# Optimization experiments

Hardware: AMD Instinct MI355X
Metric: run time of the kernel (lower is better)

Reference implementation:

```python
import jax, jax.numpy as jnp
import numpy as np

NUM_HEAD = 4
HIDDEN = 128
NEG = 9e15


def _mha(x, maskf, wq, bq, wk, bk, wv, bv, wo, bo):
    # DGN-style multi-head attention: relu on q/k/v projections, mask-multiplied
    # scores with -9e15 fill on masked entries, relu on output projection.
    bs, n, _ = x.shape
    dh = HIDDEN // NUM_HEAD
    def proj(w, b):
        return jax.nn.relu(x @ w.T + b).reshape(bs, n, NUM_HEAD, dh).transpose(0, 2, 1, 3)
    q, k, v = proj(wq, bq), proj(wk, bk), proj(wv, bv)  # [bs,H,n,dh]
    scores = jnp.einsum('bhnd,bhmd->bhnm', q, k) / jnp.sqrt(jnp.asarray(dh, x.dtype))
    m = maskf[:, None]  # [bs,1,n,n]
    scores = scores * m - NEG * (1.0 - m)
    att = jax.nn.softmax(scores, axis=-1)
    out = jnp.einsum('bhnm,bhmd->bhnd', att, v).transpose(0, 2, 1, 3).reshape(bs, n, HIDDEN)
    return jax.nn.relu(out @ wo.T + bo), att


def _gru_cell(xin, h, w_ih, w_hh, b_ih, b_hh):
    gi = xin @ w_ih.T + b_ih  # [N, 3*hidden]
    gh = h @ w_hh.T + b_hh
    i_r, i_z, i_n = jnp.split(gi, 3, axis=-1)
    h_r, h_z, h_n = jnp.split(gh, 3, axis=-1)
    r = jax.nn.sigmoid(i_r + h_r)
    z = jax.nn.sigmoid(i_z + h_z)
    n = jnp.tanh(i_n + r * h_n)
    return (1.0 - z) * n + z * h


def setup_inputs() -> dict:
    key = jax.random.key(0)
    ks = jax.random.split(key, 20)
    bs, n_ant, in_dim, hd, act = 4096, 64, 64, 128, 20
    s = 0.05
    x = jax.random.normal(ks[0], (bs, n_ant, in_dim), jnp.float32)
    mask = jax.random.randint(ks[1], (bs, n_ant, n_ant), 0, 2, jnp.int32)
    eye = jnp.eye(n_ant, dtype=jnp.int32)[None]
    mask = jnp.maximum(mask, eye)  # ensure self-edges so no softmax row is fully masked
    hidden_state = jax.random.normal(ks[2], (bs, n_ant, hd), jnp.float32)
    def w(k, shape):
        return jax.random.normal(k, shape, jnp.float32) * s
    return dict(
        x=x, mask=mask, hidden_state=hidden_state,
        enc_w=w(ks[3], (hd, in_dim)), enc_b=jnp.zeros((hd,), jnp.float32),
        q1_w=w(ks[4], (hd, hd)), q1_b=jnp.zeros((hd,), jnp.float32),
        k1_w=w(ks[5], (hd, hd)), k1_b=jnp.zeros((hd,), jnp.float32),
        v1_w=w(ks[6], (hd, hd)), v1_b=jnp.zeros((hd,), jnp.float32),
        o1_w=w(ks[7], (hd, hd)), o1_b=jnp.zeros((hd,), jnp.float32),
        q2_w=w(ks[8], (hd, hd)), q2_b=jnp.zeros((hd,), jnp.float32),
        k2_w=w(ks[9], (hd, hd)), k2_b=jnp.zeros((hd,), jnp.float32),
        v2_w=w(ks[10], (hd, hd)), v2_b=jnp.zeros((hd,), jnp.float32),
        o2_w=w(ks[11], (hd, hd)), o2_b=jnp.zeros((hd,), jnp.float32),
        gru_w_ih=w(ks[12], (3 * hd, hd)), gru_w_hh=w(ks[13], (3 * hd, hd)),
        gru_b_ih=jnp.zeros((3 * hd,), jnp.float32), gru_b_hh=jnp.zeros((3 * hd,), jnp.float32),
        lin_w=w(ks[14], (act, hd)), lin_b=jnp.zeros((act,), jnp.float32),
    )


def reference(x, mask, hidden_state,
              enc_w, enc_b,
              q1_w, q1_b, k1_w, k1_b, v1_w, v1_b, o1_w, o1_b,
              q2_w, q2_b, k2_w, k2_b, v2_w, v2_b, o2_w, o2_b,
              gru_w_ih, gru_w_hh, gru_b_ih, gru_b_hh,
              lin_w, lin_b):
    bs, n_ant, _ = x.shape
    maskf = mask.astype(x.dtype)
    xe = jax.nn.relu(x @ enc_w.T + enc_b)                     # [bs,n,hidden]
    h1, _ = _mha(xe, maskf, q1_w, q1_b, k1_w, k1_b, v1_w, v1_b, o1_w, o1_b)
    h2, _ = _mha(h1, maskf, q2_w, q2_b, k2_w, k2_b, v2_w, v2_b, o2_w, o2_b)
    h2f = h2.reshape(bs * n_ant, HIDDEN)
    hf = hidden_state.reshape(bs * n_ant, HIDDEN)
    h3 = _gru_cell(h2f, hf, gru_w_ih, gru_w_hh, gru_b_ih, gru_b_hh).reshape(bs, n_ant, HIDDEN)
    qs = h3 @ lin_w.T + lin_b                                 # with_non_linearity=False
    return qs, h3
```

## Files before the change

kernel.cpp:

```cpp
#include <hip/hip_runtime.h>
#include <hip/hip_bf16.h>

typedef unsigned int u32;
typedef unsigned short u16;
typedef unsigned long long u64;

using bf16x8 = __attribute__((ext_vector_type(8))) short;
using f32x4  = __attribute__((ext_vector_type(4))) float;
typedef float f4v __attribute__((ext_vector_type(4)));

#define NUNITS 31
#define WS_BIAS_OFF (NUNITS*8192)
#define NBIAS 1952

__device__ __forceinline__ u32 pk2(float a, float b){
    __hip_bfloat162 h = __float22bfloat162_rn(make_float2(a, b));
    union { __hip_bfloat162 h2; u32 u; } cv; cv.h2 = h; return cv.u;
}
__device__ __forceinline__ float b2f(u16 v){ return __uint_as_float(((u32)v) << 16); }
__device__ __forceinline__ int swch(int chunk, int key){ return (chunk & ~7) | ((chunk ^ key) & 7); }

__global__ __launch_bounds__(256) void convert_weights(
    const float* __restrict__ enc_w,
    const float* __restrict__ q1, const float* __restrict__ k1,
    const float* __restrict__ v1, const float* __restrict__ o1,
    const float* __restrict__ q2, const float* __restrict__ k2,
    const float* __restrict__ v2, const float* __restrict__ o2,
    const float* __restrict__ gih, const float* __restrict__ ghh,
    const float* __restrict__ lin,
    const float* __restrict__ enc_b,
    const float* __restrict__ q1b, const float* __restrict__ k1b,
    const float* __restrict__ v1b, const float* __restrict__ o1b,
    const float* __restrict__ q2b, const float* __restrict__ k2b,
    const float* __restrict__ v2b, const float* __restrict__ o2b,
    const float* __restrict__ gbih, const float* __restrict__ gbhh,
    const float* __restrict__ linb,
    u16* __restrict__ dst)
{
    int idx = blockIdx.x*256 + threadIdx.x;
    if (idx < NUNITS*8192){
        int u = idx >> 13, rem = idx & 8191;
        int w = rem >> 11;
        int t = (rem >> 9) & 3;
        int l = (rem >> 3) & 63;
        int e = idx & 7;
        int i = t >> 1, kk = t & 1;
        int oc = (w*2 + i)*16 + (l & 15);
        int kl = kk*32 + (l >> 4)*8 + e;
        float val;
        if (u == 0){
            val = enc_w[oc*64 + kl];
        } else if (u <= 16){
            int v = u - 1; int L = v >> 3; int r8 = v & 7;
            int mat, kh;
            if (r8 < 6){ mat = r8 % 3; kh = r8 / 3; } else { mat = 3; kh = r8 - 6; }
            const float* s;
            if (L == 0){ s = (mat==0)?q1:(mat==1)?k1:(mat==2)?v1:o1; }
            else       { s = (mat==0)?q2:(mat==1)?k2:(mat==2)?v2:o2; }
            val = s[oc*128 + kh*64 + kl];
        } else if (u <= 28){
            int v = u - 17;
            int gate, kh; const float* s;
            if (v < 8){ gate = v & 1; kh = (v >> 1) & 1; s = (v >= 4) ? ghh : gih; }
            else      { int w8 = v - 8; gate = 2; kh = w8 & 1; s = (w8 >= 2) ? ghh : gih; }
            val = s[(gate*128 + oc)*128 + kh*64 + kl];
        } else {
            int kh = u - 29;
            val = (oc < 20) ? lin[oc*128 + kh*64 + kl] : 0.f;
        }
        __hip_bfloat16 hv = __float2bfloat16(val);
        union { __hip_bfloat16 h; u16 us; } cv; cv.h = hv;
        dst[idx] = cv.us;
    } else if (idx < NUNITS*8192 + NBIAS){
        int i = idx - NUNITS*8192;
        float val;
        if      (i < 128)  val = enc_b[i];
        else if (i < 256)  val = q1b[i-128];
        else if (i < 384)  val = k1b[i-256];
        else if (i < 512)  val = v1b[i-384];
        else if (i < 640)  val = o1b[i-512];
        else if (i < 768)  val = q2b[i-640];
        else if (i < 896)  val = k2b[i-768];
        else if (i < 1024) val = v2b[i-896];
        else if (i < 1152) val = o2b[i-1024];
        else if (i < 1536) val = gbih[i-1152];
        else if (i < 1920) val = gbhh[i-1536];
        else if (i < 1940) val = linb[i-1920];
        else               val = 0.f;
        ((float*)(dst + NUNITS*8192))[i] = val;
    }
}

#define BARX() do{ asm volatile("s_waitcnt lgkmcnt(0)" ::: "memory"); \
                   __builtin_amdgcn_s_barrier(); \
                   asm volatile("" ::: "memory"); }while(0)

struct WB { bf16x8 a[4]; };

template<int U>
__device__ __forceinline__ WB load_unit(const u16* Wu, int w, int lane){
    const u16* p = Wu + U*8192 + w*2048 + lane*8;
    WB b;
    b.a[0] = *(const bf16x8*)(p);
    b.a[1] = *(const bf16x8*)(p + 512);
    b.a[2] = *(const bf16x8*)(p + 1024);
    b.a[3] = *(const bf16x8*)(p + 1536);
    return b;
}

template<int M,int N>
__device__ __forceinline__ void zacc(f32x4 (&a)[M][N]){
    #pragma unroll
    for (int i=0;i<M;i++)
        #pragma unroll
        for (int j=0;j<N;j++) a[i][j] = (f32x4){0.f,0.f,0.f,0.f};
}

struct XF { bf16x8 f[4][2]; };

__device__ __forceinline__ void loadX(XF& xf, const u16* X, int kh, int c, int g){
    const int key = c & 7;
    #pragma unroll
    for (int kk = 0; kk < 2; kk++){
        const int pw = (kk*4 + g) ^ key;
        #pragma unroll
        for (int j = 0; j < 4; j++)
            xf.f[j][kk] = *(const bf16x8*)(X + (j*16 + c)*128 + (kh*8 + pw)*8);
    }
}

__device__ __forceinline__ void wgemmW(const WB& wb, const XF& xf, f32x4 (&acc)[2][4]){
    __builtin_amdgcn_s_setprio(1);
    #pragma unroll
    for (int kk = 0; kk < 2; kk++){
        #pragma unroll
        for (int j = 0; j < 4; j++){
            acc[0][j] = __builtin_amdgcn_mfma_f32_16x16x32_bf16(wb.a[kk],   xf.f[j][kk], acc[0][j], 0,0,0);
            acc[1][j] = __builtin_amdgcn_mfma_f32_16x16x32_bf16(wb.a[2+kk], xf.f[j][kk], acc[1][j], 0,0,0);
        }
    }
    __builtin_amdgcn_s_setprio(0);
}

__device__ __forceinline__ void vgemmW(const WB& wb, const XF& xf, f32x4 (&acc)[4][2]){
    __builtin_amdgcn_s_setprio(1);
    #pragma unroll
    for (int kk = 0; kk < 2; kk++){
        #pragma unroll
        for (int i = 0; i < 4; i++){
            acc[i][0] = __builtin_amdgcn_mfma_f32_16x16x32_bf16(xf.f[i][kk], wb.a[kk],   acc[i][0], 0,0,0);
            acc[i][1] = __builtin_amdgcn_mfma_f32_16x16x32_bf16(xf.f[i][kk], wb.a[2+kk], acc[i][1], 0,0,0);
        }
    }
    __builtin_amdgcn_s_setprio(0);
}

__device__ __forceinline__ void epiW(f32x4 (&acc)[2][4], float4 bv0, float4 bv1,
                                     u16* dst, int w, int c, int g){
    const int key = c & 7;
    #pragma unroll
    for (int i = 0; i < 2; i++){
        float4 bv = i ? bv1 : bv0;
        const int col0 = (w*2+i)*16 + g*4;
        const int coff = swch(col0>>3, key)*8 + (col0&7);
        #pragma unroll
        for (int j = 0; j < 4; j++){
            int row = j*16 + c;
            float v0 = fmaxf(acc[i][j][0]+bv.x, 0.f);
            float v1 = fmaxf(acc[i][j][1]+bv.y, 0.f);
            float v2 = fmaxf(acc[i][j][2]+bv.z, 0.f);
            float v3 = fmaxf(acc[i][j][3]+bv.w, 0.f);
            uint2 o; o.x = pk2(v0,v1); o.y = pk2(v2,v3);
            *(uint2*)(dst + row*128 + coff) = o;
        }
    }
}

template<int LAYER>
__device__ __forceinline__ void mha_layer(const u16* Wu,
                                          u16* ACT, u16* QXp, u16* KPp,
                                          const float* wsb, const float* h0, size_t rowbase,
                                          int tid, int w, int lane, int c, int g, const u64* mbits)
{
    constexpr int UB = 1 + LAYER*8;
    constexpr int BB = 128 + LAYER*512;
    const int key = c & 7;
    const int col00 = w*32 + g*4;
    const int col01 = col00 + 16;

    XF xf;
    f32x4 accQ[2][4], accK[2][4];
    f32x4 vacc[4][2];

    WB b_q0 = load_unit<UB+0>(Wu, w, lane);
    WB b_k0 = load_unit<UB+1>(Wu, w, lane);
    WB b_v0 = load_unit<UB+2>(Wu, w, lane);

    zacc(accQ); zacc(accK); zacc(vacc);
    loadX(xf, ACT, 0, c, g);
    wgemmW(b_q0, xf, accQ);
    WB b_q1 = load_unit<UB+3>(Wu, w, lane);
    wgemmW(b_k0, xf, accK);
    WB b_k1 = load_unit<UB+4>(Wu, w, lane);
    vgemmW(b_v0, xf, vacc);
    WB b_v1 = load_unit<UB+5>(Wu, w, lane);

    loadX(xf, ACT, 1, c, g);
    float4 bq0 = *(const float4*)(wsb + BB + col00);
    float4 bq1 = *(const float4*)(wsb + BB + col01);
    wgemmW(b_q1, xf, accQ);
    WB b_o0 = load_unit<UB+6>(Wu, w, lane);
    epiW(accQ, bq0, bq1, QXp, w, c, g);

    float4 bk0 = *(const float4*)(wsb + BB + 128 + col00);
    float4 bk1 = *(const float4*)(wsb + BB + 128 + col01);
    wgemmW(b_k1, xf, accK);
    WB b_o1 = load_unit<UB+7>(Wu, w, lane);
    epiW(accK, bk0, bk1, KPp, w, c, g);

    float bv0 = wsb[BB + 256 + w*32 + c];
    float bv1 = wsb[BB + 256 + w*32 + 16 + c];
    vgemmW(b_v1, xf, vacc);

    BARX();

    #pragma unroll
    for (int j = 0; j < 2; j++){
        int vrow = w*32 + j*16 + c;
        float bv = j ? bv1 : bv0;
        #pragma unroll
        for (int i = 0; i < 4; i++){
            int kk = i >> 1, p = i & 1;
            float v0 = fmaxf(vacc[i][j][0]+bv, 0.f);
            float v1 = fmaxf(vacc[i][j][1]+bv, 0.f);
            float v2 = fmaxf(vacc[i][j][2]+bv, 0.f);
            float v3 = fmaxf(vacc[i][j][3]+bv, 0.f);
            uint2 o; o.x = pk2(v0,v1); o.y = pk2(v2,v3);
            *(uint2*)(ACT + vrow*64 + swch(kk*4+g, key)*8 + p*4) = o;
        }
    }

    const int h = w;
    f32x4 sc[4][4];
    {
        bf16x8 kf[4];
        #pragma unroll
        for (int kt = 0; kt < 4; kt++)
            kf[kt] = *(const bf16x8*)(KPp + (kt*16 + c)*128 + swch(h*4+g, key)*8);
        __builtin_amdgcn_s_setprio(1);
        #pragma unroll
        for (int qt = 0; qt < 4; qt++){
            bf16x8 qf = *(const bf16x8*)(QXp + (qt*16 + c)*128 + swch(h*4+g, key)*8);
            #pragma unroll
            for (int kt = 0; kt < 4; kt++){
                f32x4 z4 = (f32x4){0.f,0.f,0.f,0.f};
                sc[qt][kt] = __builtin_amdgcn_mfma_f32_16x16x32_bf16(kf[kt], qf, z4, 0,0,0);
            }
        }
        __builtin_amdgcn_s_setprio(0);
    }

    f4v hr[8];
    if (LAYER == 1){
        const float* hp = h0 + (rowbase + (tid>>2))*128 + (tid&3)*32;
        #pragma unroll
        for (int t = 0; t < 8; t++)
            hr[t] = __builtin_nontemporal_load((const f4v*)(hp + t*4));
    }

    {
        u32 pp[4][4][2];
        #pragma unroll
        for (int qt = 0; qt < 4; qt++){
            u64 mb = mbits[qt];
            float mx = -1e30f;
            #pragma unroll
            for (int kt = 0; kt < 4; kt++)
                #pragma unroll
                for (int r = 0; r < 4; r++){
                    float s = sc[qt][kt][r] * 0.17677669529663687f;
                    s = ((mb >> (kt*16 + g*4 + r)) & 1ull) ? s : -1e30f;
                    sc[qt][kt][r] = s;
                    mx = fmaxf(mx, s);
                }
            mx = fmaxf(mx, __shfl_xor(mx, 16));
            mx = fmaxf(mx, __shfl_xor(mx, 32));
            float sum = 0.f;
            #pragma unroll
            for (int kt = 0; kt < 4; kt++)
                #pragma unroll
                for (int r = 0; r < 4; r++){
                    float e = __expf(sc[qt][kt][r] - mx);
                    sc[qt][kt][r] = e; sum += e;
                }
            sum += __shfl_xor(sum, 16);
            sum += __shfl_xor(sum, 32);
            float inv = 1.f / sum;
            #pragma unroll
            for (int kt = 0; kt < 4; kt++){
                pp[qt][kt][0] = pk2(sc[qt][kt][0]*inv, sc[qt][kt][1]*inv);
                pp[qt][kt][1] = pk2(sc[qt][kt][2]*inv, sc[qt][kt][3]*inv);
            }
        }
        #pragma unroll
        for (int dt = 0; dt < 2; dt++){
            f32x4 pa[4];
            #pragma unroll
            for (int qt = 0; qt < 4; qt++) pa[qt] = (f32x4){0.f,0.f,0.f,0.f};
            #pragma unroll
            for (int kk = 0; kk < 2; kk++){
                bf16x8 vt = *(const bf16x8*)(ACT + (h*32 + dt*16 + c)*64 + ((kk*4+g)^key)*8);
                __builtin_amdgcn_s_setprio(1);
                #pragma unroll
                for (int qt = 0; qt < 4; qt++){
                    union { u32 u4[4]; bf16x8 v8; } bbv;
                    bbv.u4[0]=pp[qt][kk*2][0];   bbv.u4[1]=pp[qt][kk*2][1];
                    bbv.u4[2]=pp[qt][kk*2+1][0]; bbv.u4[3]=pp[qt][kk*2+1][1];
                    pa[qt] = __builtin_amdgcn_mfma_f32_16x16x32_bf16(vt, bbv.v8, pa[qt], 0,0,0);
                }
                __builtin_amdgcn_s_setprio(0);
            }
            #pragma unroll
            for (int qt = 0; qt < 4; qt++){
                int col = h*32 + dt*16 + g*4;
                uint2 o; o.x = pk2(pa[qt][0], pa[qt][1]); o.y = pk2(pa[qt][2], pa[qt][3]);
                *(uint2*)(QXp + (qt*16 + c)*128 + swch(col>>3, key)*8 + (col&7)) = o;
            }
        }
    }

    BARX();

    if (LAYER == 1){
        int hrow = tid >> 2, seg = tid & 3;
        #pragma unroll
        for (int cc = 0; cc < 4; cc++){
            int p = seg*4 + cc;
            int ps = (p & 8) | ((p ^ (hrow & 7)) & 7);
            f4v fa = hr[cc*2], fb = hr[cc*2+1];
            uint4 o; o.x = pk2(fa.x,fa.y); o.y = pk2(fa.z,fa.w);
            o.z = pk2(fb.x,fb.y); o.w = pk2(fb.z,fb.w);
            *(uint4*)(KPp + hrow*128 + ps*8) = o;
        }
    }

    f32x4 acc[2][4];
    zacc(acc);
    loadX(xf, QXp, 0, c, g);
    wgemmW(b_o0, xf, acc);
    WB b_n0 = load_unit<UB+8>(Wu, w, lane);
    loadX(xf, QXp, 1, c, g);
    float4 bo0 = *(const float4*)(wsb + BB + 384 + col00);
    float4 bo1 = *(const float4*)(wsb + BB + 384 + col01);
    wgemmW(b_o1, xf, acc);
    WB b_n1 = load_unit<UB+9>(Wu, w, lane);
    epiW(acc, bo0, bo1, ACT, w, c, g);
    asm volatile("" :: "v"(b_n0.a[0]), "v"(b_n1.a[0]));

    BARX();
}

__global__ __launch_bounds__(256, 2) void drgn_pipe(
    const float* __restrict__ x, const int* __restrict__ maskg,
    const float* __restrict__ h0, const u16* __restrict__ W16,
    float* __restrict__ out_qs, float* __restrict__ out_h3)
{
    __shared__ __align__(16) u16 SMEM[24576];
    u16* ACT = SMEM;
    u16* QXp = SMEM + 8192;
    u16* KPp = SMEM + 16384;

    const int tid = threadIdx.x;
    const int w = tid >> 6, lane = tid & 63;
    const int c = lane & 15, g = lane >> 4;
    const int key = c & 7;
    const size_t rowbase = (size_t)blockIdx.x * 64;
    const u16* Wu = W16;
    const float* wsb = (const float*)(W16 + WS_BIAS_OFF);
    const int col00 = w*32 + g*4;
    const int col01 = col00 + 16;

    u64* MrowT = (u64*)KPp;
    #pragma unroll 4
    for (int rr = 0; rr < 16; rr++){
        int row = w*16 + rr;
        int mv = __builtin_nontemporal_load(maskg + (rowbase + row)*64 + lane);
        u64 bits = __ballot(mv != 0);
        if (lane == 0) MrowT[row] = bits;
    }
    for (int i = tid; i < 512; i += 256){
        int row = i >> 3, p = i & 7;
        int lc = (p ^ (row & 7)) & 7;
        const float* sp = x + (rowbase + row)*64 + lc*8;
        f4v f0 = __builtin_nontemporal_load((const f4v*)sp);
        f4v f1 = __builtin_nontemporal_load((const f4v*)(sp + 4));
        uint4 o; o.x = pk2(f0.x,f0.y); o.y = pk2(f0.z,f0.w);
        o.z = pk2(f1.x,f1.y); o.w = pk2(f1.z,f1.w);
        *(uint4*)(QXp + row*128 + p*8) = o;
    }
    WB b_enc = load_unit<0>(Wu, w, lane);
    __syncthreads();
    u64 mbits[4];
    #pragma unroll
    for (int qt = 0; qt < 4; qt++) mbits[qt] = MrowT[qt*16 + c];

    {
        XF xf;
        f32x4 acc[2][4];
        float4 b0 = *(const float4*)(wsb + col00);
        float4 b1 = *(const float4*)(wsb + col01);
        zacc(acc);
        loadX(xf, QXp, 0, c, g);
        wgemmW(b_enc, xf, acc);
        epiW(acc, b0, b1, ACT, w, c, g);
    }
    BARX();

    mha_layer<0>(Wu, ACT, QXp, KPp, wsb, h0, rowbase, tid, w, lane, c, g, mbits);
    mha_layer<1>(Wu, ACT, QXp, KPp, wsb, h0, rowbase, tid, w, lane, c, g, mbits);

    XF xf;
    float rrA[2][4][4], zzA[2][4][4];
    {
        f32x4 aIr[2][4], aIz[2][4], aHr[2][4], aHz[2][4];
        WB g17 = load_unit<17>(Wu, w, lane);
        WB g18 = load_unit<18>(Wu, w, lane);
        zacc(aIr); zacc(aIz);
        loadX(xf, ACT, 0, c, g);
        wgemmW(g17, xf, aIr);
        WB g19 = load_unit<19>(Wu, w, lane);
        wgemmW(g18, xf, aIz);
        WB g20 = load_unit<20>(Wu, w, lane);
        loadX(xf, ACT, 1, c, g);
        wgemmW(g19, xf, aIr);
        WB g21 = load_unit<21>(Wu, w, lane);
        wgemmW(g20, xf, aIz);
        WB g22 = load_unit<22>(Wu, w, lane);
        zacc(aHr); zacc(aHz);
        loadX(xf, KPp, 0, c, g);
        wgemmW(g21, xf, aHr);
        WB g23 = load_unit<23>(Wu, w, lane);
        wgemmW(g22, xf, aHz);
        WB g24 = load_unit<24>(Wu, w, lane);
        loadX(xf, KPp, 1, c, g);
        wgemmW(g23, xf, aHr);
        wgemmW(g24, xf, aHz);

        float4 bir0 = *(const float4*)(wsb + 1152 + col00);
        float4 bir1 = *(const float4*)(wsb + 1152 + col01);
        float4 bhr0 = *(const float4*)(wsb + 1536 + col00);
        float4 bhr1 = *(const float4*)(wsb + 1536 + col01);
        float4 biz0 = *(const float4*)(wsb + 1152 + 128 + col00);
        float4 biz1 = *(const float4*)(wsb + 1152 + 128 + col01);
        float4 bhz0 = *(const float4*)(wsb + 1536 + 128 + col00);
        float4 bhz1 = *(const float4*)(wsb + 1536 + 128 + col01);
        #pragma unroll
        for (int i = 0; i < 2; i++){
            float4 bir = i ? bir1 : bir0; float4 bhr = i ? bhr1 : bhr0;
            float4 biz = i ? biz1 : biz0; float4 bhz = i ? bhz1 : bhz0;
            #pragma unroll
            for (int j = 0; j < 4; j++)
                #pragma unroll
                for (int r = 0; r < 4; r++){
                    rrA[i][j][r] = 1.f/(1.f + __expf(-(aIr[i][j][r] + (&bir.x)[r] + aHr[i][j][r] + (&bhr.x)[r])));
                    zzA[i][j][r] = 1.f/(1.f + __expf(-(aIz[i][j][r] + (&biz.x)[r] + aHz[i][j][r] + (&bhz.x)[r])));
                }
        }
    }
    WB g29, g30;
    {
        f32x4 aIn[2][4], aHn[2][4];
        WB g25 = load_unit<25>(Wu, w, lane);
        WB g26 = load_unit<26>(Wu, w, lane);
        zacc(aIn);
        loadX(xf, ACT, 0, c, g);
        wgemmW(g25, xf, aIn);
        WB g27 = load_unit<27>(Wu, w, lane);
        loadX(xf, ACT, 1, c, g);
        wgemmW(g26, xf, aIn);
        WB g28 = load_unit<28>(Wu, w, lane);
        zacc(aHn);
        loadX(xf, KPp, 0, c, g);
        wgemmW(g27, xf, aHn);
        g29 = load_unit<29>(Wu, w, lane);
        loadX(xf, KPp, 1, c, g);
        wgemmW(g28, xf, aHn);
        g30 = load_unit<30>(Wu, w, lane);

        float4 bin0 = *(const float4*)(wsb + 1152 + 256 + col00);
        float4 bin1 = *(const float4*)(wsb + 1152 + 256 + col01);
        float4 bhn0 = *(const float4*)(wsb + 1536 + 256 + col00);
        float4 bhn1 = *(const float4*)(wsb + 1536 + 256 + col01);

        BARX();

        #pragma unroll
        for (int i = 0; i < 2; i++){
            float4 bi = i ? bin1 : bin0; float4 bh = i ? bhn1 : bhn0;
            int col0 = w*32 + i*16 + g*4;
            int coff = swch(col0>>3, key)*8 + (col0&7);
            #pragma unroll
            for (int j = 0; j < 4; j++){
                int row = j*16 + c;
                uint2 hv = *(const uint2*)(KPp + row*128 + coff);
                float h0v[4] = { b2f((u16)(hv.x & 0xffffu)), b2f((u16)(hv.x >> 16)),
                                 b2f((u16)(hv.y & 0xffffu)), b2f((u16)(hv.y >> 16)) };
                f4v h3o;
                #pragma unroll
                for (int r = 0; r < 4; r++){
                    float xn = aIn[i][j][r] + (&bi.x)[r] + rrA[i][j][r]*(aHn[i][j][r] + (&bh.x)[r]);
                    float e2 = __expf(-2.f*fabsf(xn));
                    float th = (1.f - e2)/(1.f + e2);
                    th = (xn >= 0.f) ? th : -th;
                    float zv = zzA[i][j][r];
                    h3o[r] = (1.f - zv)*th + zv*h0v[r];
                }
                uint2 o; o.x = pk2(h3o[0],h3o[1]); o.y = pk2(h3o[2],h3o[3]);
                *(uint2*)(ACT + row*128 + coff) = o;
                __builtin_nontemporal_store(h3o, (f4v*)(out_h3 + (rowbase + row)*128 + col0));
            }
        }
    }
    BARX();

    {
        f32x4 qa[2][4];
        float4 lb0 = (col00 < 20) ? *(const float4*)(wsb + 1920 + col00) : (float4){0.f,0.f,0.f,0.f};
        float4 lb1 = (col01 < 20) ? *(const float4*)(wsb + 1920 + col01) : (float4){0.f,0.f,0.f,0.f};
        zacc(qa);
        loadX(xf, ACT, 0, c, g);
        wgemmW(g29, xf, qa);
        loadX(xf, ACT, 1, c, g);
        wgemmW(g30, xf, qa);

        #pragma unroll
        for (int i = 0; i < 2; i++){
            int col0 = w*32 + i*16 + g*4;
            if (col0 < 20){
                float4 lb = i ? lb1 : lb0;
                #pragma unroll
                for (int j = 0; j < 4; j++){
                    int row = j*16 + c;
                    f4v o;
                    o.x = qa[i][j][0]+lb.x; o.y = qa[i][j][1]+lb.y;
                    o.z = qa[i][j][2]+lb.z; o.w = qa[i][j][3]+lb.w;
                    __builtin_nontemporal_store(o, (f4v*)(out_qs + (rowbase + row)*20 + col0));
                }
            }
        }
    }
}

extern "C" void kernel_launch(void* const* d_in, const int* in_sizes, int n_in,
                              void* d_out, int out_size, void* d_ws, size_t ws_size,
                              hipStream_t stream) {
    const float* x     = (const float*)d_in[0];
    const int*   mask  = (const int*)  d_in[1];
    const float* h0    = (const float*)d_in[2];
    const float* enc_w = (const float*)d_in[3];
    const float* enc_b = (const float*)d_in[4];
    const float* q1_w  = (const float*)d_in[5];  const float* q1_b = (const float*)d_in[6];
    const float* k1_w  = (const float*)d_in[7];  const float* k1_b = (const float*)d_in[8];
    const float* v1_w  = (const float*)d_in[9];  const float* v1_b = (const float*)d_in[10];
    const float* o1_w  = (const float*)d_in[11]; const float* o1_b = (const float*)d_in[12];
    const float* q2_w  = (const float*)d_in[13]; const float* q2_b = (const float*)d_in[14];
    const float* k2_w  = (const float*)d_in[15]; const float* k2_b = (const float*)d_in[16];
    const float* v2_w  = (const float*)d_in[17]; const float* v2_b = (const float*)d_in[18];
    const float* o2_w  = (const float*)d_in[19]; const float* o2_b = (const float*)d_in[20];
    const float* gwih  = (const float*)d_in[21]; const float* gwhh = (const float*)d_in[22];
    const float* gbih  = (const float*)d_in[23]; const float* gbhh = (const float*)d_in[24];
    const float* lin_w = (const float*)d_in[25]; const float* lin_b = (const float*)d_in[26];

    const int bs = in_sizes[0] / (64 * 64);
    float* out_qs = (float*)d_out;
    float* out_h3 = out_qs + (size_t)bs * 64 * 20;
    u16* W16 = (u16*)d_ws;

    const int total = NUNITS*8192 + NBIAS;
    hipLaunchKernelGGL(convert_weights, dim3((total + 255) / 256), dim3(256), 0, stream,
                       enc_w, q1_w, k1_w, v1_w, o1_w, q2_w, k2_w, v2_w, o2_w,
                       gwih, gwhh, lin_w,
                       enc_b, q1_b, k1_b, v1_b, o1_b, q2_b, k2_b, v2_b, o2_b,
                       gbih, gbhh, lin_b, W16);
    hipLaunchKernelGGL(drgn_pipe, dim3(bs), dim3(256), 0, stream,
                       x, mask, h0, W16, out_qs, out_h3);
}
```

Baseline: 328.8 us.

## Prefetch next-layer weights across stages, fold softmax scale, use fast exp2/rcp

Weight units for the next stage (layer 1 QKV, GRU first units) are now loaded at the end of the previous stage and passed through, so global weight latency overlaps the preceding GEMMs. The softmax drops the max-subtraction pass by pre-scaling Q with scale*log2e and using exp2 directly, and normalization is deferred to after the PV matmul. Sigmoid/tanh use hardware exp2 and rcp intrinsics, and MFMA accumulator zeroing is folded into the first MFMA. Skipping max subtraction risks overflow if scores grow large, and the held prefetched weights raise register pressure.

```diff
diff --git a/kernel.cpp b/kernel.cpp
--- a/kernel.cpp
+++ b/kernel.cpp
@@ -12,6 +12,8 @@
 #define NUNITS 31
 #define WS_BIAS_OFF (NUNITS*8192)
 #define NBIAS 1952
+#define SCL2 0.25503512f
+#define L2E  1.4426950408889634f
 
 __device__ __forceinline__ u32 pk2(float a, float b){
     __hip_bfloat162 h = __float22bfloat162_rn(make_float2(a, b));
@@ -19,6 +21,9 @@
 }
 __device__ __forceinline__ float b2f(u16 v){ return __uint_as_float(((u32)v) << 16); }
 __device__ __forceinline__ int swch(int chunk, int key){ return (chunk & ~7) | ((chunk ^ key) & 7); }
+__device__ __forceinline__ float sigx(float v){
+    return __builtin_amdgcn_rcpf(1.f + __builtin_amdgcn_exp2f(-L2E * v));
+}
 
 __global__ __launch_bounds__(256) void convert_weights(
     const float* __restrict__ enc_w,
@@ -108,13 +113,8 @@
     return b;
 }
 
-template<int M,int N>
-__device__ __forceinline__ void zacc(f32x4 (&a)[M][N]){
-    #pragma unroll
-    for (int i=0;i<M;i++)
-        #pragma unroll
-        for (int j=0;j<N;j++) a[i][j] = (f32x4){0.f,0.f,0.f,0.f};
-}
+#define Z4 ((f32x4){0.f,0.f,0.f,0.f})
+#define MFMA(a,b,c) __builtin_amdgcn_mfma_f32_16x16x32_bf16((a),(b),(c),0,0,0)
 
 struct XF { bf16x8 f[4][2]; };
 
@@ -129,32 +129,39 @@
     }
 }
 
+template<bool FIRST>
 __device__ __forceinline__ void wgemmW(const WB& wb, const XF& xf, f32x4 (&acc)[2][4]){
     __builtin_amdgcn_s_setprio(1);
     #pragma unroll
-    for (int kk = 0; kk < 2; kk++){
-        #pragma unroll
-        for (int j = 0; j < 4; j++){
-            acc[0][j] = __builtin_amdgcn_mfma_f32_16x16x32_bf16(wb.a[kk],   xf.f[j][kk], acc[0][j], 0,0,0);
-            acc[1][j] = __builtin_amdgcn_mfma_f32_16x16x32_bf16(wb.a[2+kk], xf.f[j][kk], acc[1][j], 0,0,0);
-        }
+    for (int j = 0; j < 4; j++){
+        acc[0][j] = FIRST ? MFMA(wb.a[0], xf.f[j][0], Z4) : MFMA(wb.a[0], xf.f[j][0], acc[0][j]);
+        acc[1][j] = FIRST ? MFMA(wb.a[2], xf.f[j][0], Z4) : MFMA(wb.a[2], xf.f[j][0], acc[1][j]);
+    }
+    #pragma unroll
+    for (int j = 0; j < 4; j++){
+        acc[0][j] = MFMA(wb.a[1], xf.f[j][1], acc[0][j]);
+        acc[1][j] = MFMA(wb.a[3], xf.f[j][1], acc[1][j]);
     }
     __builtin_amdgcn_s_setprio(0);
 }
 
+template<bool FIRST>
 __device__ __forceinline__ void vgemmW(const WB& wb, const XF& xf, f32x4 (&acc)[4][2]){
     __builtin_amdgcn_s_setprio(1);
     #pragma unroll
-    for (int kk = 0; kk < 2; kk++){
-        #pragma unroll
-        for (int i = 0; i < 4; i++){
-            acc[i][0] = __builtin_amdgcn_mfma_f32_16x16x32_bf16(xf.f[i][kk], wb.a[kk],   acc[i][0], 0,0,0);
-            acc[i][1] = __builtin_amdgcn_mfma_f32_16x16x32_bf16(xf.f[i][kk], wb.a[2+kk], acc[i][1], 0,0,0);
-        }
+    for (int i = 0; i < 4; i++){
+        acc[i][0] = FIRST ? MFMA(xf.f[i][0], wb.a[0], Z4) : MFMA(xf.f[i][0], wb.a[0], acc[i][0]);
+        acc[i][1] = FIRST ? MFMA(xf.f[i][0], wb.a[2], Z4) : MFMA(xf.f[i][0], wb.a[2], acc[i][1]);
+    }
+    #pragma unroll
+    for (int i = 0; i < 4; i++){
+        acc[i][0] = MFMA(xf.f[i][1], wb.a[1], acc[i][0]);
+        acc[i][1] = MFMA(xf.f[i][1], wb.a[3], acc[i][1]);
     }
     __builtin_amdgcn_s_setprio(0);
 }
 
+template<bool QS>
 __device__ __forceinline__ void epiW(f32x4 (&acc)[2][4], float4 bv0, float4 bv1,
                                      u16* dst, int w, int c, int g){
     const int key = c & 7;
@@ -170,6 +177,7 @@
             float v1 = fmaxf(acc[i][j][1]+bv.y, 0.f);
             float v2 = fmaxf(acc[i][j][2]+bv.z, 0.f);
             float v3 = fmaxf(acc[i][j][3]+bv.w, 0.f);
+            if (QS){ v0 *= SCL2; v1 *= SCL2; v2 *= SCL2; v3 *= SCL2; }
             uint2 o; o.x = pk2(v0,v1); o.y = pk2(v2,v3);
             *(uint2*)(dst + row*128 + coff) = o;
         }
@@ -180,7 +188,9 @@
 __device__ __forceinline__ void mha_layer(const u16* Wu,
                                           u16* ACT, u16* QXp, u16* KPp,
                                           const float* wsb, const float* h0, size_t rowbase,
-                                          int tid, int w, int lane, int c, int g, const u64* mbits)
+                                          int tid, int w, int lane, int c, int g, const u64* mbits,
+                                          WB b_q0, WB b_k0, WB b_v0,
+                                          WB& nx0, WB& nx1, WB& nx2)
 {
     constexpr int UB = 1 + LAYER*8;
     constexpr int BB = 128 + LAYER*512;
@@ -192,35 +202,30 @@
     f32x4 accQ[2][4], accK[2][4];
     f32x4 vacc[4][2];
 
-    WB b_q0 = load_unit<UB+0>(Wu, w, lane);
-    WB b_k0 = load_unit<UB+1>(Wu, w, lane);
-    WB b_v0 = load_unit<UB+2>(Wu, w, lane);
-
-    zacc(accQ); zacc(accK); zacc(vacc);
     loadX(xf, ACT, 0, c, g);
-    wgemmW(b_q0, xf, accQ);
+    wgemmW<true>(b_q0, xf, accQ);
     WB b_q1 = load_unit<UB+3>(Wu, w, lane);
-    wgemmW(b_k0, xf, accK);
+    wgemmW<true>(b_k0, xf, accK);
     WB b_k1 = load_unit<UB+4>(Wu, w, lane);
-    vgemmW(b_v0, xf, vacc);
+    vgemmW<true>(b_v0, xf, vacc);
     WB b_v1 = load_unit<UB+5>(Wu, w, lane);
 
     loadX(xf, ACT, 1, c, g);
     float4 bq0 = *(const float4*)(wsb + BB + col00);
     float4 bq1 = *(const float4*)(wsb + BB + col01);
-    wgemmW(b_q1, xf, accQ);
+    wgemmW<false>(b_q1, xf, accQ);
     WB b_o0 = load_unit<UB+6>(Wu, w, lane);
-    epiW(accQ, bq0, bq1, QXp, w, c, g);
+    epiW<true>(accQ, bq0, bq1, QXp, w, c, g);
 
     float4 bk0 = *(const float4*)(wsb + BB + 128 + col00);
     float4 bk1 = *(const float4*)(wsb + BB + 128 + col01);
-    wgemmW(b_k1, xf, accK);
+    wgemmW<false>(b_k1, xf, accK);
     WB b_o1 = load_unit<UB+7>(Wu, w, lane);
-    epiW(accK, bk0, bk1, KPp, w, c, g);
+    epiW<false>(accK, bk0, bk1, KPp, w, c, g);
 
     float bv0 = wsb[BB + 256 + w*32 + c];
     float bv1 = wsb[BB + 256 + w*32 + 16 + c];
-    vgemmW(b_v1, xf, vacc);
+    vgemmW<false>(b_v1, xf, vacc);
 
     BARX();
 
@@ -252,10 +257,8 @@
         for (int qt = 0; qt < 4; qt++){
             bf16x8 qf = *(const bf16x8*)(QXp + (qt*16 + c)*128 + swch(h*4+g, key)*8);
             #pragma unroll
-            for (int kt = 0; kt < 4; kt++){
-                f32x4 z4 = (f32x4){0.f,0.f,0.f,0.f};
-                sc[qt][kt] = __builtin_amdgcn_mfma_f32_16x16x32_bf16(kf[kt], qf, z4, 0,0,0);
-            }
+            for (int kt = 0; kt < 4; kt++)
+                sc[qt][kt] = MFMA(kf[kt], qf, Z4);
         }
         __builtin_amdgcn_s_setprio(0);
     }
@@ -270,43 +273,31 @@
 
     {
         u32 pp[4][4][2];
+        float inv[4];
         #pragma unroll
         for (int qt = 0; qt < 4; qt++){
             u64 mb = mbits[qt];
-            float mx = -1e30f;
+            float sum = 0.f;
             #pragma unroll
             for (int kt = 0; kt < 4; kt++)
                 #pragma unroll
                 for (int r = 0; r < 4; r++){
-                    float s = sc[qt][kt][r] * 0.17677669529663687f;
-                    s = ((mb >> (kt*16 + g*4 + r)) & 1ull) ? s : -1e30f;
-                    sc[qt][kt][r] = s;
-                    mx = fmaxf(mx, s);
-                }
-            mx = fmaxf(mx, __shfl_xor(mx, 16));
-            mx = fmaxf(mx, __shfl_xor(mx, 32));
-            float sum = 0.f;
-            #pragma unroll
-            for (int kt = 0; kt < 4; kt++)
-                #pragma unroll
-                for (int r = 0; r < 4; r++){
-                    float e = __expf(sc[qt][kt][r] - mx);
+                    float s = ((mb >> (kt*16 + g*4 + r)) & 1ull) ? sc[qt][kt][r] : -1e30f;
+                    float e = __builtin_amdgcn_exp2f(s);
                     sc[qt][kt][r] = e; sum += e;
                 }
             sum += __shfl_xor(sum, 16);
             sum += __shfl_xor(sum, 32);
-            float inv = 1.f / sum;
+            inv[qt] = __builtin_amdgcn_rcpf(sum);
             #pragma unroll
             for (int kt = 0; kt < 4; kt++){
-                pp[qt][kt][0] = pk2(sc[qt][kt][0]*inv, sc[qt][kt][1]*inv);
-                pp[qt][kt][1] = pk2(sc[qt][kt][2]*inv, sc[qt][kt][3]*inv);
+                pp[qt][kt][0] = pk2(sc[qt][kt][0], sc[qt][kt][1]);
+                pp[qt][kt][1] = pk2(sc[qt][kt][2], sc[qt][kt][3]);
             }
         }
         #pragma unroll
         for (int dt = 0; dt < 2; dt++){
             f32x4 pa[4];
-            #pragma unroll
-            for (int qt = 0; qt < 4; qt++) pa[qt] = (f32x4){0.f,0.f,0.f,0.f};
             #pragma unroll
             for (int kk = 0; kk < 2; kk++){
                 bf16x8 vt = *(const bf16x8*)(ACT + (h*32 + dt*16 + c)*64 + ((kk*4+g)^key)*8);
@@ -316,14 +307,15 @@
                     union { u32 u4[4]; bf16x8 v8; } bbv;
                     bbv.u4[0]=pp[qt][kk*2][0];   bbv.u4[1]=pp[qt][kk*2][1];
                     bbv.u4[2]=pp[qt][kk*2+1][0]; bbv.u4[3]=pp[qt][kk*2+1][1];
-                    pa[qt] = __builtin_amdgcn_mfma_f32_16x16x32_bf16(vt, bbv.v8, pa[qt], 0,0,0);
+                    pa[qt] = (kk == 0) ? MFMA(vt, bbv.v8, Z4) : MFMA(vt, bbv.v8, pa[qt]);
                 }
                 __builtin_amdgcn_s_setprio(0);
             }
             #pragma unroll
             for (int qt = 0; qt < 4; qt++){
                 int col = h*32 + dt*16 + g*4;
-                uint2 o; o.x = pk2(pa[qt][0], pa[qt][1]); o.y = pk2(pa[qt][2], pa[qt][3]);
+                float iv = inv[qt];
+                uint2 o; o.x = pk2(pa[qt][0]*iv, pa[qt][1]*iv); o.y = pk2(pa[qt][2]*iv, pa[qt][3]*iv);
                 *(uint2*)(QXp + (qt*16 + c)*128 + swch(col>>3, key)*8 + (col&7)) = o;
             }
         }
@@ -345,17 +337,16 @@
     }
 
     f32x4 acc[2][4];
-    zacc(acc);
     loadX(xf, QXp, 0, c, g);
-    wgemmW(b_o0, xf, acc);
-    WB b_n0 = load_unit<UB+8>(Wu, w, lane);
+    wgemmW<true>(b_o0, xf, acc);
+    nx0 = load_unit<UB+8>(Wu, w, lane);
+    nx1 = load_unit<UB+9>(Wu, w, lane);
     loadX(xf, QXp, 1, c, g);
     float4 bo0 = *(const float4*)(wsb + BB + 384 + col00);
     float4 bo1 = *(const float4*)(wsb + BB + 384 + col01);
-    wgemmW(b_o1, xf, acc);
-    WB b_n1 = load_unit<UB+9>(Wu, w, lane);
-    epiW(acc, bo0, bo1, ACT, w, c, g);
-    asm volatile("" :: "v"(b_n0.a[0]), "v"(b_n1.a[0]));
+    wgemmW<false>(b_o1, xf, acc);
+    nx2 = load_unit<UB+10>(Wu, w, lane);
+    epiW<false>(acc, bo0, bo1, ACT, w, c, g);
 
     BARX();
 }
@@ -399,6 +390,9 @@
         *(uint4*)(QXp + row*128 + p*8) = o;
     }
     WB b_enc = load_unit<0>(Wu, w, lane);
+    WB n0 = load_unit<1>(Wu, w, lane);
+    WB n1 = load_unit<2>(Wu, w, lane);
+    WB n2 = load_unit<3>(Wu, w, lane);
     __syncthreads();
     u64 mbits[4];
     #pragma unroll
@@ -409,42 +403,42 @@
         f32x4 acc[2][4];
         float4 b0 = *(const float4*)(wsb + col00);
         float4 b1 = *(const float4*)(wsb + col01);
-        zacc(acc);
         loadX(xf, QXp, 0, c, g);
-        wgemmW(b_enc, xf, acc);
-        epiW(acc, b0, b1, ACT, w, c, g);
+        wgemmW<true>(b_enc, xf, acc);
+        epiW<false>(acc, b0, b1, ACT, w, c, g);
     }
     BARX();
 
-    mha_layer<0>(Wu, ACT, QXp, KPp, wsb, h0, rowbase, tid, w, lane, c, g, mbits);
-    mha_layer<1>(Wu, ACT, QXp, KPp, wsb, h0, rowbase, tid, w, lane, c, g, mbits);
+    mha_layer<0>(Wu, ACT, QXp, KPp, wsb, h0, rowbase, tid, w, lane, c, g, mbits,
+                 n0, n1, n2, n0, n1, n2);
+    mha_layer<1>(Wu, ACT, QXp, KPp, wsb, h0, rowbase, tid, w, lane, c, g, mbits,
+                 n0, n1, n2, n0, n1, n2);
 
     XF xf;
     float rrA[2][4][4], zzA[2][4][4];
+    WB g29, g30;
     {
         f32x4 aIr[2][4], aIz[2][4], aHr[2][4], aHz[2][4];
-        WB g17 = load_unit<17>(Wu, w, lane);
-        WB g18 = load_unit<18>(Wu, w, lane);
-        zacc(aIr); zacc(aIz);
         loadX(xf, ACT, 0, c, g);
-        wgemmW(g17, xf, aIr);
-        WB g19 = load_unit<19>(Wu, w, lane);
-        wgemmW(g18, xf, aIz);
+        wgemmW<true>(n0, xf, aIr);
         WB g20 = load_unit<20>(Wu, w, lane);
+        wgemmW<true>(n1, xf, aIz);
+        WB g21 = load_unit<21>(Wu, w, lane);
         loadX(xf, ACT, 1, c, g);
-        wgemmW(g19, xf, aIr);
-        WB g21 = load_unit<21>(Wu, w, lane);
-        wgemmW(g20, xf, aIz);
+        wgemmW<false>(n2, xf, aIr);
         WB g22 = load_unit<22>(Wu, w, lane);
-        zacc(aHr); zacc(aHz);
+        wgemmW<false>(g20, xf, aIz);
+        WB g23 = load_unit<23>(Wu, w, lane);
         loadX(xf, KPp, 0, c, g);
-        wgemmW(g21, xf, aHr);
-        WB g23 = load_unit<23>(Wu, w, lane);
-        wgemmW(g22, xf, aHz);
+        wgemmW<true>(g21, xf, aHr);
         WB g24 = load_unit<24>(Wu, w, lane);
+        wgemmW<true>(g22, xf, aHz);
+        WB g25 = load_unit<25>(Wu, w, lane);
         loadX(xf, KPp, 1, c, g);
-        wgemmW(g23, xf, aHr);
-        wgemmW(g24, xf, aHz);
+        wgemmW<false>(g23, xf, aHr);
+        WB g26 = load_unit<26>(Wu, w, lane);
+        wgemmW<false>(g24, xf, aHz);
+        WB g27 = load_unit<27>(Wu, w, lane);
 
         float4 bir0 = *(const float4*)(wsb + 1152 + col00);
         float4 bir1 = *(const float4*)(wsb + 1152 + col01);
@@ -462,30 +456,23 @@
             for (int j = 0; j < 4; j++)
                 #pragma unroll
                 for (int r = 0; r < 4; r++){
-                    rrA[i][j][r] = 1.f/(1.f + __expf(-(aIr[i][j][r] + (&bir.x)[r] + aHr[i][j][r] + (&bhr.x)[r])));
-                    zzA[i][j][r] = 1.f/(1.f + __expf(-(aIz[i][j][r] + (&biz.x)[r] + aHz[i][j][r] + (&bhz.x)[r])));
+                    rrA[i][j][r] = sigx(aIr[i][j][r] + (&bir.x)[r] + aHr[i][j][r] + (&bhr.x)[r]);
+                    zzA[i][j][r] = sigx(aIz[i][j][r] + (&biz.x)[r] + aHz[i][j][r] + (&bhz.x)[r]);
                 }
         }
-    }
-    WB g29, g30;
-    {
+
         f32x4 aIn[2][4], aHn[2][4];
-        WB g25 = load_unit<25>(Wu, w, lane);
-        WB g26 = load_unit<26>(Wu, w, lane);
-        zacc(aIn);
         loadX(xf, ACT, 0, c, g);
-        wgemmW(g25, xf, aIn);
-        WB g27 = load_unit<27>(Wu, w, lane);
+        wgemmW<true>(g25, xf, aIn);
+        WB g28 = load_unit<28>(Wu, w, lane);
         loadX(xf, ACT, 1, c, g);
-        wgemmW(g26, xf, aIn);
-        WB g28 = load_unit<28>(Wu, w, lane);
-        zacc(aHn);
+        wgemmW<false>(g26, xf, aIn);
+        g29 = load_unit<29>(Wu, w, lane);
         loadX(xf, KPp, 0, c, g);
-        wgemmW(g27, xf, aHn);
-        g29 = load_unit<29>(Wu, w, lane);
+        wgemmW<true>(g27, xf, aHn);
+        g30 = load_unit<30>(Wu, w, lane);
         loadX(xf, KPp, 1, c, g);
-        wgemmW(g28, xf, aHn);
-        g30 = load_unit<30>(Wu, w, lane);
+        wgemmW<false>(g28, xf, aHn);
 
         float4 bin0 = *(const float4*)(wsb + 1152 + 256 + col00);
         float4 bin1 = *(const float4*)(wsb + 1152 + 256 + col01);
@@ -509,8 +496,8 @@
                 #pragma unroll
                 for (int r = 0; r < 4; r++){
                     float xn = aIn[i][j][r] + (&bi.x)[r] + rrA[i][j][r]*(aHn[i][j][r] + (&bh.x)[r]);
-                    float e2 = __expf(-2.f*fabsf(xn));
-                    float th = (1.f - e2)/(1.f + e2);
+                    float e2 = __builtin_amdgcn_exp2f(-2.f*L2E*fabsf(xn));
+                    float th = (1.f - e2)*__builtin_amdgcn_rcpf(1.f + e2);
                     th = (xn >= 0.f) ? th : -th;
                     float zv = zzA[i][j][r];
                     h3o[r] = (1.f - zv)*th + zv*h0v[r];
@@ -527,11 +514,10 @@
         f32x4 qa[2][4];
         float4 lb0 = (col00 < 20) ? *(const float4*)(wsb + 1920 + col00) : (float4){0.f,0.f,0.f,0.f};
         float4 lb1 = (col01 < 20) ? *(const float4*)(wsb + 1920 + col01) : (float4){0.f,0.f,0.f,0.f};
-        zacc(qa);
         loadX(xf, ACT, 0, c, g);
-        wgemmW(g29, xf, qa);
+        wgemmW<true>(g29, xf, qa);
         loadX(xf, ACT, 1, c, g);
-        wgemmW(g30, xf, qa);
+        wgemmW<false>(g30, xf, qa);
 
         #pragma unroll
         for (int i = 0; i < 2; i++){
```

Result: faster. 313.1 us (-4.8%).
